# Kernel optimization log

Hardware: AMD Instinct MI355X
Metric: run time of the kernel (lower is better)

Reference implementation:

```python
import jax, jax.numpy as jnp
import numpy as np

B, N, M, C1, C2 = 4, 8192, 2048, 128, 256
H1, H2 = 256, 128  # mlp = [C2+C1, 256, 128]
EPS_DIST = 1e-8
EPS_BN = 1e-5
K = 3


def setup_inputs() -> dict:
    key = jax.random.key(0)
    ks = jax.random.split(key, 6)
    return {
        "unknown": jax.random.normal(ks[0], (B, N, 3), dtype=jnp.float32),
        "known": jax.random.normal(ks[1], (B, M, 3), dtype=jnp.float32),
        "unknow_feats": jax.random.normal(ks[2], (B, C1, N), dtype=jnp.float32),
        "known_feats": jax.random.normal(ks[3], (B, C2, M), dtype=jnp.float32),
        "W1": jax.random.normal(ks[4], (H1, C1 + C2), dtype=jnp.float32) * 0.05,
        "g1": jnp.ones((H1,), jnp.float32),
        "b1": jnp.zeros((H1,), jnp.float32),
        "W2": jax.random.normal(ks[5], (H2, H1), dtype=jnp.float32) * 0.05,
        "g2": jnp.ones((H2,), jnp.float32),
        "b2": jnp.zeros((H2,), jnp.float32),
    }


def _bn_relu(x, g, b):
    # training-mode BatchNorm over (batch, spatial) axes for (B, C, N) tensor
    mean = jnp.mean(x, axis=(0, 2), keepdims=True)
    var = jnp.var(x, axis=(0, 2), keepdims=True)
    y = (x - mean) * jax.lax.rsqrt(var + EPS_BN) * g[None, :, None] + b[None, :, None]
    return jax.nn.relu(y)


def reference(unknown, known, unknow_feats, known_feats, W1, g1, b1, W2, g2, b2):
    # 3-NN: squared euclidean distances (B, N, M) via expansion (avoids B,N,M,3 temp)
    d2 = (
        jnp.sum(unknown * unknown, axis=-1)[:, :, None]
        + jnp.sum(known * known, axis=-1)[:, None, :]
        - 2.0 * jnp.einsum("bnc,bmc->bnm", unknown, known)
    )
    neg_d, idx = jax.lax.top_k(-d2, K)  # smallest-K squared dists
    dist = -neg_d  # (B, N, K), squared distances (pytorch3d knn_points convention)
    recip = 1.0 / (dist + EPS_DIST)
    weight = recip / jnp.sum(recip, axis=2, keepdims=True)  # (B, N, K)

    kf = jnp.swapaxes(known_feats, 1, 2)  # (B, M, C2)
    grouped = jax.vmap(lambda f, i: f[i])(kf, idx)  # (B, N, K, C2)
    interp = jnp.einsum("bnkc,bnk->bcn", grouped, weight)  # (B, C2, N)

    x = jnp.concatenate([interp, unknow_feats], axis=1)  # (B, C2+C1, N)
    x = _bn_relu(jnp.einsum("oc,bcn->bon", W1, x), g1, b1)
    x = _bn_relu(jnp.einsum("oc,bcn->bon", W2, x), g2, b2)
    return x  # (B, H2, N)
```

## Files before the change

### kernel.cpp

```cpp
#include <hip/hip_runtime.h>
#include <hip/hip_bf16.h>
#include <cstdint>
#include <cstddef>

typedef unsigned short u16;
typedef __attribute__((ext_vector_type(8))) short bf16x8;
typedef __attribute__((ext_vector_type(4))) float f32x4;

constexpr int Bn = 4;
constexpr int Nq = 8192;
constexpr int Mk = 2048;
constexpr int C1c = 128;
constexpr int C2c = 256;
constexpr int H1c = 256;
constexpr int H2c = 128;

__device__ __forceinline__ float bf2f(u16 u) {
    union { uint32_t i; float f; } v;
    v.i = (uint32_t)u << 16;
    return v.f;
}
__device__ __forceinline__ u16 f2bf(float f) {
    const uint32_t x = __float_as_uint(f);
    return (u16)((x + 0x7FFFu + ((x >> 16) & 1u)) >> 16);
}
__device__ __forceinline__ uint32_t cvtpk(float lo, float hi) {
    uint32_t r;
    asm("v_cvt_pk_bf16_f32 %0, %1, %2" : "=v"(r) : "v"(lo), "v"(hi));
    return r;
}

__global__ __launch_bounds__(256) void knn_prep_kernel(
    const float* __restrict__ W1, const float* __restrict__ W2,
    u16* __restrict__ W1b, u16* __restrict__ W2b,
    const float* __restrict__ KF, u16* __restrict__ KFt,
    const float* __restrict__ UF, u16* __restrict__ UFt,
    const float* __restrict__ unknown, const float* __restrict__ known,
    int* __restrict__ idx_out, float* __restrict__ w_out)
{
    __shared__ __align__(16) char smem[32768];
    const int bid = blockIdx.x;
    const int t = threadIdx.x;

    if (bid < 2048) {
        float4* kp = (float4*)smem;
        const int b = bid >> 9;
        const int n0 = (bid & 511) * 16;

        const float* kb = known + (size_t)b * Mk * 3;
        for (int i = t; i < Mk; i += 256) {
            const float x = kb[i * 3 + 0], y = kb[i * 3 + 1], z = kb[i * 3 + 2];
            kp[i] = make_float4(x, y, z, fmaf(x, x, fmaf(y, y, z * z)));
        }
        __syncthreads();

        const int q = n0 + (t >> 4);
        const int s = t & 15;
        const float* u = unknown + ((size_t)b * Nq + q) * 3;
        const float ux = u[0], uy = u[1], uz = u[2];
        const float nux = -2.0f * ux, nuy = -2.0f * uy, nuz = -2.0f * uz;
        const float uu = fmaf(ux, ux, fmaf(uy, uy, uz * uz));

        float d0 = 1e30f, d1 = 1e30f, d2 = 1e30f;
        int i0 = 0, i1 = 0, i2 = 0;

        auto ins = [&](float d, int i) {
            const bool c0 = d < d0, c1 = d < d1, c2 = d < d2;
            const float nd0 = fminf(d0, d);
            const float nd1 = __builtin_amdgcn_fmed3f(d0, d, d1);
            const float nd2 = __builtin_amdgcn_fmed3f(d1, d, d2);
            i2 = c1 ? i1 : (c2 ? i : i2);
            i1 = c0 ? i0 : (c1 ? i : i1);
            i0 = c0 ? i : i0;
            d0 = nd0; d1 = nd1; d2 = nd2;
        };

        #pragma unroll 8
        for (int it = 0; it < Mk / 16; ++it) {
            const int m = it * 16 + s;
            const float4 p = kp[m];
            const float d = fmaf(nux, p.x, fmaf(nuy, p.y, fmaf(nuz, p.z, p.w)));
            ins(d, m);
        }
        #pragma unroll
        for (int off = 1; off <= 8; off <<= 1) {
            const float e0 = __shfl_xor(d0, off), e1 = __shfl_xor(d1, off), e2 = __shfl_xor(d2, off);
            const int j0 = __shfl_xor(i0, off), j1 = __shfl_xor(i1, off), j2 = __shfl_xor(i2, off);
            ins(e0, j0);
            ins(e1, j1);
            ins(e2, j2);
        }
        if (s == 0) {
            const float f0 = d0 + uu, f1 = d1 + uu, f2 = d2 + uu;
            const float r0 = 1.0f / (f0 + 1e-8f);
            const float r1 = 1.0f / (f1 + 1e-8f);
            const float r2 = 1.0f / (f2 + 1e-8f);
            const float inv = 1.0f / (r0 + r1 + r2);
            const size_t base = ((size_t)b * Nq + q) * 3;
            idx_out[base + 0] = i0;
            idx_out[base + 1] = i1;
            idx_out[base + 2] = i2;
            w_out[base + 0] = r0 * inv;
            w_out[base + 1] = r1 * inv;
            w_out[base + 2] = r2 * inv;
        }
    } else if (bid < 2176) {
        const int cb = bid - 2048;
        const float* X = (cb < 96) ? W1 : W2;
        u16* Y = (cb < 96) ? W1b : W2b;
        const int i = ((cb < 96) ? cb : (cb - 96)) * 256 + t;
        const float4 v = *(const float4*)&X[(size_t)i * 4];
        ushort4 o;
        o.x = f2bf(v.x); o.y = f2bf(v.y); o.z = f2bf(v.z); o.w = f2bf(v.w);
        *(ushort4*)&Y[(size_t)i * 4] = o;
    } else {
        const float* X;
        u16* Y;
        int C, M, m0, c0;
        if (bid < 2688) {
            const int f = bid - 2176;
            const int b = f >> 7, rem = f & 127;
            C = C2c; M = Mk; m0 = (rem >> 2) * 64; c0 = (rem & 3) * 64;
            X = KF + (size_t)b * C * M;
            Y = KFt + (size_t)b * M * C;
        } else {
            const int f = bid - 2688;
            const int b = f >> 8, rem = f & 255;
            C = C1c; M = Nq; m0 = (rem >> 1) * 64; c0 = (rem & 1) * 64;
            X = UF + (size_t)b * C * M;
            Y = UFt + (size_t)b * M * C;
        }
        float (*T)[65] = (float(*)[65])smem;
        const int m4 = (t & 15) * 4, cr = t >> 4;
        #pragma unroll
        for (int i = 0; i < 4; ++i) {
            const float4 v = *(const float4*)&X[(size_t)(c0 + cr + i * 16) * M + m0 + m4];
            T[cr + i * 16][m4 + 0] = v.x;
            T[cr + i * 16][m4 + 1] = v.y;
            T[cr + i * 16][m4 + 2] = v.z;
            T[cr + i * 16][m4 + 3] = v.w;
        }
        __syncthreads();
        const int c4 = (t & 15) * 4, mr = t >> 4;
        #pragma unroll
        for (int i = 0; i < 4; ++i) {
            const int m = mr + i * 16;
            ushort4 o;
            o.x = f2bf(T[c4 + 0][m]);
            o.y = f2bf(T[c4 + 1][m]);
            o.z = f2bf(T[c4 + 2][m]);
            o.w = f2bf(T[c4 + 3][m]);
            *(ushort4*)&Y[(size_t)(m0 + m) * C + c0 + c4] = o;
        }
    }
}

__device__ __forceinline__ uint4 bnx(uint4 x, const float* scs, const float* bis, int k) {
    const u16* p = (const u16*)&x;
    const float4 s0 = *(const float4*)&scs[k];
    const float4 s1 = *(const float4*)&scs[k + 4];
    const float4 b0 = *(const float4*)&bis[k];
    const float4 b1 = *(const float4*)&bis[k + 4];
    const float* sa = (const float*)&s0;
    const float* sb = (const float*)&s1;
    const float* ba = (const float*)&b0;
    const float* bb = (const float*)&b1;
    uint4 o;
    uint32_t* po = (uint32_t*)&o;
    #pragma unroll
    for (int w2 = 0; w2 < 2; ++w2) {
        const float a0 = fmaxf(0.0f, fmaf(bf2f(p[2 * w2 + 0]), sa[2 * w2 + 0], ba[2 * w2 + 0]));
        const float a1 = fmaxf(0.0f, fmaf(bf2f(p[2 * w2 + 1]), sa[2 * w2 + 1], ba[2 * w2 + 1]));
        po[w2] = cvtpk(a0, a1);
    }
    #pragma unroll
    for (int w2 = 0; w2 < 2; ++w2) {
        const float a0 = fmaxf(0.0f, fmaf(bf2f(p[4 + 2 * w2 + 0]), sb[2 * w2 + 0], bb[2 * w2 + 0]));
        const float a1 = fmaxf(0.0f, fmaf(bf2f(p[4 + 2 * w2 + 1]), sb[2 * w2 + 1], bb[2 * w2 + 1]));
        po[2 + w2] = cvtpk(a0, a1);
    }
    return o;
}

template <int GATHER, int OUT_BF16, int STATS, int BNIN>
__global__ __launch_bounds__(256) void mfma_gemm(
    const u16* __restrict__ A, int lda, size_t sA,
    const u16* __restrict__ Bt, int ldb, size_t sB,
    void* __restrict__ Cout, int ldc, size_t sC,
    int nK,
    const u16* __restrict__ Ptb,
    const int* __restrict__ idx, const float* __restrict__ wgt, int nrows,
    const float* __restrict__ bn_s, const float* __restrict__ bn_b,
    float* __restrict__ partS, float* __restrict__ partQ)
{
    __shared__ u16 As[4096];
    __shared__ u16 Bs[4096];
    __shared__ float scs[256], bis[256];
    __shared__ float sS[2][128], sQ[2][128];

    const int b = blockIdx.z;
    const int m0 = blockIdx.x * 128, n0 = blockIdx.y * 128;
    const int t = threadIdx.x;
    const int l = t & 63, wv = t >> 6;
    const int wr = wv >> 1, wc = wv & 1;

    if (BNIN) {
        scs[t] = bn_s[t];
        bis[t] = bn_b[t];
    }

    const u16* Ab = A + (size_t)b * sA;
    const u16* Btb = Bt + (size_t)b * sB;
    const int rA0 = t >> 2, rA1 = (t + 256) >> 2;
    const int ko = (t & 3) * 8;

    f32x4 acc[4][4];
    const f32x4 z = {0.0f, 0.0f, 0.0f, 0.0f};
    #pragma unroll
    for (int i = 0; i < 4; ++i)
        #pragma unroll
        for (int j = 0; j < 4; ++j) acc[i][j] = z;

    uint4 a0 = *(const uint4*)&Ab[(size_t)(m0 + rA0) * lda + ko];
    uint4 a1 = *(const uint4*)&Ab[(size_t)(m0 + rA1) * lda + ko];
    uint4 b0 = *(const uint4*)&Btb[(size_t)(n0 + rA0) * ldb + ko];
    uint4 b1 = *(const uint4*)&Btb[(size_t)(n0 + rA1) * ldb + ko];
    if (BNIN) __syncthreads();

    for (int kt = 0; kt < nK; ++kt) {
        *(uint4*)&As[t * 8] = a0;
        *(uint4*)&As[(t + 256) * 8] = a1;
        if (BNIN) {
            const int k = kt * 32 + ko;
            *(uint4*)&Bs[t * 8] = bnx(b0, scs, bis, k);
            *(uint4*)&Bs[(t + 256) * 8] = bnx(b1, scs, bis, k);
        } else {
            *(uint4*)&Bs[t * 8] = b0;
            *(uint4*)&Bs[(t + 256) * 8] = b1;
        }
        __syncthreads();
        if (kt + 1 < nK) {
            const int k0 = (kt + 1) * 32;
            a0 = *(const uint4*)&Ab[(size_t)(m0 + rA0) * lda + k0 + ko];
            a1 = *(const uint4*)&Ab[(size_t)(m0 + rA1) * lda + k0 + ko];
            b0 = *(const uint4*)&Btb[(size_t)(n0 + rA0) * ldb + k0 + ko];
            b1 = *(const uint4*)&Btb[(size_t)(n0 + rA1) * ldb + k0 + ko];
        }
        bf16x8 af[4], bf[4];
        #pragma unroll
        for (int f = 0; f < 4; ++f) {
            af[f] = *(const bf16x8*)&As[(wr * 64 + f * 16 + (l & 15)) * 32 + (l >> 4) * 8];
            bf[f] = *(const bf16x8*)&Bs[(wc * 64 + f * 16 + (l & 15)) * 32 + (l >> 4) * 8];
        }
        #pragma unroll
        for (int i = 0; i < 4; ++i)
            #pragma unroll
            for (int j = 0; j < 4; ++j)
                acc[i][j] = __builtin_amdgcn_mfma_f32_16x16x32_bf16(af[i], bf[j], acc[i][j], 0, 0, 0);
        __syncthreads();
    }

    const int cb = l & 15;
    const int rg = (l >> 4) * 4;
    float sj[4] = {0, 0, 0, 0}, qj[4] = {0, 0, 0, 0};
    #pragma unroll
    for (int i = 0; i < 4; ++i) {
        #pragma unroll
        for (int r = 0; r < 4; ++r) {
            const int R = m0 + wr * 64 + i * 16 + rg + r;
            const u16 *P0 = nullptr, *P1 = nullptr, *P2 = nullptr;
            float w0 = 0.0f, w1 = 0.0f, w2 = 0.0f;
            if (GATHER) {
                const size_t ib = ((size_t)b * nrows + R) * 3;
                const int j0 = idx[ib], j1 = idx[ib + 1], j2 = idx[ib + 2];
                w0 = wgt[ib];
                w1 = wgt[ib + 1];
                w2 = wgt[ib + 2];
                const u16* Pb = Ptb + (size_t)b * Mk * 256;
                P0 = Pb + (size_t)j0 * 256;
                P1 = Pb + (size_t)j1 * 256;
                P2 = Pb + (size_t)j2 * 256;
            }
            #pragma unroll
            for (int j = 0; j < 4; ++j) {
                const int Cc = n0 + wc * 64 + j * 16 + cb;
                float v = acc[i][j][r];
                if (GATHER)
                    v += w0 * bf2f(P0[Cc]) + w1 * bf2f(P1[Cc]) + w2 * bf2f(P2[Cc]);
                if (OUT_BF16)
                    ((u16*)Cout)[(size_t)b * sC + (size_t)R * ldc + Cc] = f2bf(v);
                else
                    ((float*)Cout)[(size_t)b * sC + (size_t)R * ldc + Cc] = v;
                if (STATS == 1) {
                    sj[j] += v;
                    qj[j] += v * v;
                }
                if (STATS == 2) acc[i][j][r] = v;
            }
        }
    }

    if (STATS == 1) {
        #pragma unroll
        for (int j = 0; j < 4; ++j) {
            float s = sj[j], q = qj[j];
            s += __shfl_xor(s, 16); s += __shfl_xor(s, 32);
            q += __shfl_xor(q, 16); q += __shfl_xor(q, 32);
            if (l < 16) {
                sS[wr][wc * 64 + j * 16 + l] = s;
                sQ[wr][wc * 64 + j * 16 + l] = q;
            }
        }
        __syncthreads();
        if (t < 128) {
            const float S = sS[0][t] + sS[1][t];
            const float Q = sQ[0][t] + sQ[1][t];
            const int pblk = blockIdx.z * gridDim.x + blockIdx.x;
            partS[(size_t)pblk * 256 + blockIdx.y * 128 + t] = S;
            partQ[(size_t)pblk * 256 + blockIdx.y * 128 + t] = Q;
        }
    }
    if (STATS == 2) {
        #pragma unroll
        for (int i = 0; i < 4; ++i) {
            #pragma unroll
            for (int r = 0; r < 4; ++r) {
                float s = acc[i][0][r] + acc[i][1][r] + acc[i][2][r] + acc[i][3][r];
                float q = acc[i][0][r] * acc[i][0][r] + acc[i][1][r] * acc[i][1][r] +
                          acc[i][2][r] * acc[i][2][r] + acc[i][3][r] * acc[i][3][r];
                s += __shfl_xor(s, 1); s += __shfl_xor(s, 2);
                s += __shfl_xor(s, 4); s += __shfl_xor(s, 8);
                q += __shfl_xor(q, 1); q += __shfl_xor(q, 2);
                q += __shfl_xor(q, 4); q += __shfl_xor(q, 8);
                if ((l & 15) == 0) {
                    const int row = wr * 64 + i * 16 + (l >> 4) * 4 + r;
                    sS[wc][row] = s;
                    sQ[wc][row] = q;
                }
            }
        }
        __syncthreads();
        if (t < 128) {
            const float S = sS[0][t] + sS[1][t];
            const float Q = sQ[0][t] + sQ[1][t];
            const int pblk = blockIdx.z * gridDim.y + blockIdx.y;
            partS[(size_t)pblk * 128 + t] = S;
            partQ[(size_t)pblk * 128 + t] = Q;
        }
    }
}

__global__ __launch_bounds__(1024) void bn_finalize(
    const float* __restrict__ pS, const float* __restrict__ pQ,
    const float* __restrict__ g, const float* __restrict__ beta,
    float* __restrict__ scale, float* __restrict__ bias,
    int C, int np, float cnt)
{
    __shared__ float rs[1024], rq[1024];
    const int t = threadIdx.x;
    const int c = t & (C - 1);
    const int sl = t / C;
    const int nsl = 1024 / C;
    float s = 0.0f, q = 0.0f;
    for (int i = sl; i < np; i += nsl) {
        s += pS[(size_t)i * C + c];
        q += pQ[(size_t)i * C + c];
    }
    rs[t] = s;
    rq[t] = q;
    __syncthreads();
    if (t < C) {
        for (int k = 1; k < nsl; ++k) {
            s += rs[t + k * C];
            q += rq[t + k * C];
        }
        const float mean = s / cnt;
        const float var = q / cnt - mean * mean;
        const float r = rsqrtf(var + 1e-5f);
        const float sc = g[t] * r;
        scale[t] = sc;
        bias[t] = beta[t] - mean * sc;
    }
}

__global__ __launch_bounds__(256) void bn2_apply_kernel(
    float* __restrict__ Y,
    const float* __restrict__ pS, const float* __restrict__ pQ,
    const float* __restrict__ g, const float* __restrict__ beta)
{
    __shared__ float rs[256], rq[256];
    const int t = threadIdx.x;
    const size_t base = (size_t)blockIdx.x * 1024;
    const int c = (int)((base / Nq) % H2c);

    rs[t] = pS[(size_t)t * 128 + c];
    rq[t] = pQ[(size_t)t * 128 + c];
    __syncthreads();
    for (int off = 128; off > 0; off >>= 1) {
        if (t < off) {
            rs[t] += rs[t + off];
            rq[t] += rq[t + off];
        }
        __syncthreads();
    }
    if (t == 0) {
        const float cnt = (float)(Bn * Nq);
        const float mean = rs[0] / cnt;
        const float var = rq[0] / cnt - mean * mean;
        const float r = rsqrtf(var + 1e-5f);
        const float sc = g[c] * r;
        rs[0] = sc;
        rq[0] = beta[c] - mean * sc;
    }
    __syncthreads();
    const float sc = rs[0], bi = rq[0];
    float4 v = *(float4*)&Y[base + t * 4];
    v.x = fmaxf(0.0f, fmaf(v.x, sc, bi));
    v.y = fmaxf(0.0f, fmaf(v.y, sc, bi));
    v.z = fmaxf(0.0f, fmaf(v.z, sc, bi));
    v.w = fmaxf(0.0f, fmaf(v.w, sc, bi));
    *(float4*)&Y[base + t * 4] = v;
}

extern "C" void kernel_launch(void* const* d_in, const int* in_sizes, int n_in,
                              void* d_out, int out_size, void* d_ws, size_t ws_size,
                              hipStream_t stream) {
    const float* unknown = (const float*)d_in[0];
    const float* known = (const float*)d_in[1];
    const float* unknow_feats = (const float*)d_in[2];
    const float* known_feats = (const float*)d_in[3];
    const float* W1 = (const float*)d_in[4];
    const float* g1 = (const float*)d_in[5];
    const float* b1 = (const float*)d_in[6];
    const float* W2 = (const float*)d_in[7];
    const float* g2 = (const float*)d_in[8];
    const float* b2 = (const float*)d_in[9];
    float* out = (float*)d_out;

    char* w = (char*)d_ws;
    u16* KFt = (u16*)w; w += (size_t)Bn * Mk * C2c * 2;
    u16* UFt = (u16*)w; w += (size_t)Bn * Nq * C1c * 2;
    u16* W1b = (u16*)w; w += (size_t)H1c * 384 * 2;
    u16* W2b = (u16*)w; w += (size_t)H2c * H1c * 2;
    u16* Ptb = (u16*)w; w += (size_t)Bn * Mk * H1c * 2;
    u16* y1b = (u16*)w; w += (size_t)Bn * Nq * H1c * 2;
    int* idx = (int*)w; w += (size_t)Bn * Nq * 3 * 4;
    float* wgt = (float*)w; w += (size_t)Bn * Nq * 3 * 4;
    float* pS1 = (float*)w; w += (size_t)256 * 256 * 4;
    float* pQ1 = (float*)w; w += (size_t)256 * 256 * 4;
    float* pS2 = (float*)w; w += (size_t)256 * 128 * 4;
    float* pQ2 = (float*)w; w += (size_t)256 * 128 * 4;
    float* scale1 = (float*)w; w += 1024;
    float* bias1 = (float*)w; w += 1024;

    knn_prep_kernel<<<3712, 256, 0, stream>>>(W1, W2, W1b, W2b,
                                              known_feats, KFt, unknow_feats, UFt,
                                              unknown, known, idx, wgt);

    mfma_gemm<0, 1, 0, 0><<<dim3(Mk / 128, H1c / 128, Bn), 256, 0, stream>>>(
        KFt, C2c, (size_t)Mk * C2c,
        W1b, 384, 0,
        Ptb, H1c, (size_t)Mk * H1c,
        C2c / 32, nullptr, nullptr, nullptr, 0,
        nullptr, nullptr, nullptr, nullptr);

    mfma_gemm<1, 1, 1, 0><<<dim3(Nq / 128, H1c / 128, Bn), 256, 0, stream>>>(
        UFt, C1c, (size_t)Nq * C1c,
        W1b + C2c, 384, 0,
        y1b, H1c, (size_t)Nq * H1c,
        C1c / 32, Ptb, idx, wgt, Nq,
        nullptr, nullptr, pS1, pQ1);

    bn_finalize<<<1, 1024, 0, stream>>>(pS1, pQ1, g1, b1, scale1, bias1,
                                        H1c, 256, (float)(Bn * Nq));

    mfma_gemm<0, 0, 2, 1><<<dim3(1, Nq / 128, Bn), 256, 0, stream>>>(
        W2b, H1c, 0,
        y1b, H1c, (size_t)Nq * H1c,
        out, Nq, (size_t)H2c * Nq,
        H1c / 32, nullptr, nullptr, nullptr, 0,
        scale1, bias1, pS2, pQ2);

    bn2_apply_kernel<<<(Bn * H2c * Nq) / 1024, 256, 0, stream>>>(out, pS2, pQ2, g2, b2);
}
```

Baseline: 109.2 us.

## Rebalance KNN lanes per query and split second GEMM into 64-row tiles

```diff
diff --git a/kernel.cpp b/kernel.cpp
--- a/kernel.cpp
+++ b/kernel.cpp
@@ -42,10 +42,10 @@
     const int bid = blockIdx.x;
     const int t = threadIdx.x;
 
-    if (bid < 2048) {
+    if (bid < 1024) {
         float4* kp = (float4*)smem;
-        const int b = bid >> 9;
-        const int n0 = (bid & 511) * 16;
+        const int b = bid >> 8;
+        const int n0 = (bid & 255) * 32;
 
         const float* kb = known + (size_t)b * Mk * 3;
         for (int i = t; i < Mk; i += 256) {
@@ -54,8 +54,8 @@
         }
         __syncthreads();
 
-        const int q = n0 + (t >> 4);
-        const int s = t & 15;
+        const int q = n0 + (t >> 3);
+        const int s = t & 7;
         const float* u = unknown + ((size_t)b * Nq + q) * 3;
         const float ux = u[0], uy = u[1], uz = u[2];
         const float nux = -2.0f * ux, nuy = -2.0f * uy, nuz = -2.0f * uz;
@@ -76,14 +76,14 @@
         };
 
         #pragma unroll 8
-        for (int it = 0; it < Mk / 16; ++it) {
-            const int m = it * 16 + s;
+        for (int it = 0; it < Mk / 8; ++it) {
+            const int m = it * 8 + s;
             const float4 p = kp[m];
             const float d = fmaf(nux, p.x, fmaf(nuy, p.y, fmaf(nuz, p.z, p.w)));
             ins(d, m);
         }
         #pragma unroll
-        for (int off = 1; off <= 8; off <<= 1) {
+        for (int off = 1; off <= 4; off <<= 1) {
             const float e0 = __shfl_xor(d0, off), e1 = __shfl_xor(d1, off), e2 = __shfl_xor(d2, off);
             const int j0 = __shfl_xor(i0, off), j1 = __shfl_xor(i1, off), j2 = __shfl_xor(i2, off);
             ins(e0, j0);
@@ -104,8 +104,8 @@
             w_out[base + 1] = r1 * inv;
             w_out[base + 2] = r2 * inv;
         }
-    } else if (bid < 2176) {
-        const int cb = bid - 2048;
+    } else if (bid < 1152) {
+        const int cb = bid - 1024;
         const float* X = (cb < 96) ? W1 : W2;
         u16* Y = (cb < 96) ? W1b : W2b;
         const int i = ((cb < 96) ? cb : (cb - 96)) * 256 + t;
@@ -117,14 +117,14 @@
         const float* X;
         u16* Y;
         int C, M, m0, c0;
-        if (bid < 2688) {
-            const int f = bid - 2176;
+        if (bid < 1664) {
+            const int f = bid - 1152;
             const int b = f >> 7, rem = f & 127;
             C = C2c; M = Mk; m0 = (rem >> 2) * 64; c0 = (rem & 3) * 64;
             X = KF + (size_t)b * C * M;
             Y = KFt + (size_t)b * M * C;
         } else {
-            const int f = bid - 2688;
+            const int f = bid - 1664;
             const int b = f >> 8, rem = f & 255;
             C = C1c; M = Nq; m0 = (rem >> 1) * 64; c0 = (rem & 1) * 64;
             X = UF + (size_t)b * C * M;
@@ -182,20 +182,18 @@
     return o;
 }
 
-template <int GATHER, int OUT_BF16, int STATS, int BNIN>
+template <int GATHER, int STATS>
 __global__ __launch_bounds__(256) void mfma_gemm(
     const u16* __restrict__ A, int lda, size_t sA,
     const u16* __restrict__ Bt, int ldb, size_t sB,
-    void* __restrict__ Cout, int ldc, size_t sC,
+    u16* __restrict__ Cout, int ldc, size_t sC,
     int nK,
     const u16* __restrict__ Ptb,
     const int* __restrict__ idx, const float* __restrict__ wgt, int nrows,
-    const float* __restrict__ bn_s, const float* __restrict__ bn_b,
     float* __restrict__ partS, float* __restrict__ partQ)
 {
     __shared__ u16 As[4096];
     __shared__ u16 Bs[4096];
-    __shared__ float scs[256], bis[256];
     __shared__ float sS[2][128], sQ[2][128];
 
     const int b = blockIdx.z;
@@ -204,11 +202,6 @@
     const int l = t & 63, wv = t >> 6;
     const int wr = wv >> 1, wc = wv & 1;
 
-    if (BNIN) {
-        scs[t] = bn_s[t];
-        bis[t] = bn_b[t];
-    }
-
     const u16* Ab = A + (size_t)b * sA;
     const u16* Btb = Bt + (size_t)b * sB;
     const int rA0 = t >> 2, rA1 = (t + 256) >> 2;
@@ -225,19 +218,12 @@
     uint4 a1 = *(const uint4*)&Ab[(size_t)(m0 + rA1) * lda + ko];
     uint4 b0 = *(const uint4*)&Btb[(size_t)(n0 + rA0) * ldb + ko];
     uint4 b1 = *(const uint4*)&Btb[(size_t)(n0 + rA1) * ldb + ko];
-    if (BNIN) __syncthreads();
 
     for (int kt = 0; kt < nK; ++kt) {
         *(uint4*)&As[t * 8] = a0;
         *(uint4*)&As[(t + 256) * 8] = a1;
-        if (BNIN) {
-            const int k = kt * 32 + ko;
-            *(uint4*)&Bs[t * 8] = bnx(b0, scs, bis, k);
-            *(uint4*)&Bs[(t + 256) * 8] = bnx(b1, scs, bis, k);
-        } else {
-            *(uint4*)&Bs[t * 8] = b0;
-            *(uint4*)&Bs[(t + 256) * 8] = b1;
-        }
+        *(uint4*)&Bs[t * 8] = b0;
+        *(uint4*)&Bs[(t + 256) * 8] = b1;
         __syncthreads();
         if (kt + 1 < nK) {
             const int k0 = (kt + 1) * 32;
@@ -287,20 +273,16 @@
                 float v = acc[i][j][r];
                 if (GATHER)
                     v += w0 * bf2f(P0[Cc]) + w1 * bf2f(P1[Cc]) + w2 * bf2f(P2[Cc]);
-                if (OUT_BF16)
-                    ((u16*)Cout)[(size_t)b * sC + (size_t)R * ldc + Cc] = f2bf(v);
-                else
-                    ((float*)Cout)[(size_t)b * sC + (size_t)R * ldc + Cc] = v;
-                if (STATS == 1) {
+                Cout[(size_t)b * sC + (size_t)R * ldc + Cc] = f2bf(v);
+                if (STATS) {
                     sj[j] += v;
                     qj[j] += v * v;
                 }
-                if (STATS == 2) acc[i][j][r] = v;
             }
         }
     }
 
-    if (STATS == 1) {
+    if (STATS) {
         #pragma unroll
         for (int j = 0; j < 4; ++j) {
             float s = sj[j], q = qj[j];
@@ -320,33 +302,107 @@
             partQ[(size_t)pblk * 256 + blockIdx.y * 128 + t] = Q;
         }
     }
-    if (STATS == 2) {
-        #pragma unroll
-        for (int i = 0; i < 4; ++i) {
+}
+
+__global__ __launch_bounds__(256) void mfma_gemm3(
+    const u16* __restrict__ W2b,
+    const u16* __restrict__ Y,
+    float* __restrict__ out,
+    const float* __restrict__ bn_s, const float* __restrict__ bn_b,
+    float* __restrict__ partS, float* __restrict__ partQ)
+{
+    __shared__ u16 As[2048];
+    __shared__ u16 Bs[4096];
+    __shared__ float scs[256], bis[256];
+    __shared__ float sS[2][64], sQ[2][64];
+
+    const int b = blockIdx.z;
+    const int m0 = blockIdx.x * 64;
+    const int n0 = blockIdx.y * 128;
+    const int t = threadIdx.x;
+    const int l = t & 63, wv = t >> 6;
+    const int wr = wv >> 1, wc = wv & 1;
+
+    scs[t] = bn_s[t];
+    bis[t] = bn_b[t];
+
+    const u16* Yb = Y + (size_t)b * Nq * 256;
+    const int rA = t >> 2;
+    const int rB1 = (t + 256) >> 2;
+    const int ko = (t & 3) * 8;
+
+    f32x4 acc[2][4];
+    const f32x4 z = {0.0f, 0.0f, 0.0f, 0.0f};
+    #pragma unroll
+    for (int i = 0; i < 2; ++i)
+        #pragma unroll
+        for (int j = 0; j < 4; ++j) acc[i][j] = z;
+
+    uint4 a0 = *(const uint4*)&W2b[(size_t)(m0 + rA) * 256 + ko];
+    uint4 b0 = *(const uint4*)&Yb[(size_t)(n0 + rA) * 256 + ko];
+    uint4 b1 = *(const uint4*)&Yb[(size_t)(n0 + rB1) * 256 + ko];
+    __syncthreads();
+
+    for (int kt = 0; kt < 8; ++kt) {
+        const int k = kt * 32 + ko;
+        *(uint4*)&As[t * 8] = a0;
+        *(uint4*)&Bs[t * 8] = bnx(b0, scs, bis, k);
+        *(uint4*)&Bs[(t + 256) * 8] = bnx(b1, scs, bis, k);
+        __syncthreads();
+        if (kt + 1 < 8) {
+            const int k0 = (kt + 1) * 32;
+            a0 = *(const uint4*)&W2b[(size_t)(m0 + rA) * 256 + k0 + ko];
+            b0 = *(const uint4*)&Yb[(size_t)(n0 + rA) * 256 + k0 + ko];
+            b1 = *(const uint4*)&Yb[(size_t)(n0 + rB1) * 256 + k0 + ko];
+        }
+        bf16x8 af[2], bf[4];
+        #pragma unroll
+        for (int f = 0; f < 2; ++f)
+            af[f] = *(const bf16x8*)&As[(wr * 32 + f * 16 + (l & 15)) * 32 + (l >> 4) * 8];
+        #pragma unroll
+        for (int f = 0; f < 4; ++f)
+            bf[f] = *(const bf16x8*)&Bs[(wc * 64 + f * 16 + (l & 15)) * 32 + (l >> 4) * 8];
+        #pragma unroll
+        for (int i = 0; i < 2; ++i)
             #pragma unroll
-            for (int r = 0; r < 4; ++r) {
-                float s = acc[i][0][r] + acc[i][1][r] + acc[i][2][r] + acc[i][3][r];
-                float q = acc[i][0][r] * acc[i][0][r] + acc[i][1][r] * acc[i][1][r] +
-                          acc[i][2][r] * acc[i][2][r] + acc[i][3][r] * acc[i][3][r];
-                s += __shfl_xor(s, 1); s += __shfl_xor(s, 2);
-                s += __shfl_xor(s, 4); s += __shfl_xor(s, 8);
-                q += __shfl_xor(q, 1); q += __shfl_xor(q, 2);
-                q += __shfl_xor(q, 4); q += __shfl_xor(q, 8);
-                if ((l & 15) == 0) {
-                    const int row = wr * 64 + i * 16 + (l >> 4) * 4 + r;
-                    sS[wc][row] = s;
-                    sQ[wc][row] = q;
-                }
+            for (int j = 0; j < 4; ++j)
+                acc[i][j] = __builtin_amdgcn_mfma_f32_16x16x32_bf16(af[i], bf[j], acc[i][j], 0, 0, 0);
+        __syncthreads();
+    }
+
+    const int cb = l & 15;
+    const int rg = (l >> 4) * 4;
+    float* ob = out + (size_t)b * H2c * Nq;
+    #pragma unroll
+    for (int i = 0; i < 2; ++i) {
+        #pragma unroll
+        for (int r = 0; r < 4; ++r) {
+            const int Rl = wr * 32 + i * 16 + rg + r;
+            #pragma unroll
+            for (int j = 0; j < 4; ++j) {
+                const int Cc = n0 + wc * 64 + j * 16 + cb;
+                ob[(size_t)(m0 + Rl) * Nq + Cc] = acc[i][j][r];
             }
-        }
-        __syncthreads();
-        if (t < 128) {
-            const float S = sS[0][t] + sS[1][t];
-            const float Q = sQ[0][t] + sQ[1][t];
-            const int pblk = blockIdx.z * gridDim.y + blockIdx.y;
-            partS[(size_t)pblk * 128 + t] = S;
-            partQ[(size_t)pblk * 128 + t] = Q;
-        }
+            float s = acc[i][0][r] + acc[i][1][r] + acc[i][2][r] + acc[i][3][r];
+            float q = acc[i][0][r] * acc[i][0][r] + acc[i][1][r] * acc[i][1][r] +
+                      acc[i][2][r] * acc[i][2][r] + acc[i][3][r] * acc[i][3][r];
+            s += __shfl_xor(s, 1); s += __shfl_xor(s, 2);
+            s += __shfl_xor(s, 4); s += __shfl_xor(s, 8);
+            q += __shfl_xor(q, 1); q += __shfl_xor(q, 2);
+            q += __shfl_xor(q, 4); q += __shfl_xor(q, 8);
+            if ((l & 15) == 0) {
+                sS[wc][Rl] = s;
+                sQ[wc][Rl] = q;
+            }
+        }
+    }
+    __syncthreads();
+    if (t < 64) {
+        const float S = sS[0][t] + sS[1][t];
+        const float Q = sQ[0][t] + sQ[1][t];
+        const int p = blockIdx.z * gridDim.y + blockIdx.y;
+        partS[(size_t)p * 128 + m0 + t] = S;
+        partQ[(size_t)p * 128 + m0 + t] = Q;
     }
 }
 
@@ -453,33 +509,27 @@
     float* scale1 = (float*)w; w += 1024;
     float* bias1 = (float*)w; w += 1024;
 
-    knn_prep_kernel<<<3712, 256, 0, stream>>>(W1, W2, W1b, W2b,
+    knn_prep_kernel<<<2688, 256, 0, stream>>>(W1, W2, W1b, W2b,
                                               known_feats, KFt, unknow_feats, UFt,
                                               unknown, known, idx, wgt);
 
-    mfma_gemm<0, 1, 0, 0><<<dim3(Mk / 128, H1c / 128, Bn), 256, 0, stream>>>(
+    mfma_gemm<0, 0><<<dim3(Mk / 128, H1c / 128, Bn), 256, 0, stream>>>(
         KFt, C2c, (size_t)Mk * C2c,
         W1b, 384, 0,
         Ptb, H1c, (size_t)Mk * H1c,
-        C2c / 32, nullptr, nullptr, nullptr, 0,
-        nullptr, nullptr, nullptr, nullptr);
-
-    mfma_gemm<1, 1, 1, 0><<<dim3(Nq / 128, H1c / 128, Bn), 256, 0, stream>>>(
+        C2c / 32, nullptr, nullptr, nullptr, 0, nullptr, nullptr);
+
+    mfma_gemm<1, 1><<<dim3(Nq / 128, H1c / 128, Bn), 256, 0, stream>>>(
         UFt, C1c, (size_t)Nq * C1c,
         W1b + C2c, 384, 0,
         y1b, H1c, (size_t)Nq * H1c,
-        C1c / 32, Ptb, idx, wgt, Nq,
-        nullptr, nullptr, pS1, pQ1);
+        C1c / 32, Ptb, idx, wgt, Nq, pS1, pQ1);
 
     bn_finalize<<<1, 1024, 0, stream>>>(pS1, pQ1, g1, b1, scale1, bias1,
                                         H1c, 256, (float)(Bn * Nq));
 
-    mfma_gemm<0, 0, 2, 1><<<dim3(1, Nq / 128, Bn), 256, 0, stream>>>(
-        W2b, H1c, 0,
-        y1b, H1c, (size_t)Nq * H1c,
-        out, Nq, (size_t)H2c * Nq,
-        H1c / 32, nullptr, nullptr, nullptr, 0,
-        scale1, bias1, pS2, pQ2);
+    mfma_gemm3<<<dim3(2, Nq / 128, Bn), 256, 0, stream>>>(
+        W2b, y1b, out, scale1, bias1, pS2, pQ2);
 
     bn2_apply_kernel<<<(Bn * H2c * Nq) / 1024, 256, 0, stream>>>(out, pS2, pQ2, g2, b2);
 }
```

Result: faster. 104.8 us (-4.0%).
